# Optimization experiments

Hardware: AMD Instinct MI355X
Metric: run time of the kernel (lower is better)

The kernel has to match this reference:

```python
import jax, jax.numpy as jnp
import numpy as np
from math import sqrt

D_MODEL = 1024
N_HEADS = 16
D_V = D_MODEL // N_HEADS
D_FF = 4 * D_MODEL
EPS = 1e-5


def setup_inputs() -> dict:
    key = jax.random.key(0)
    ks = jax.random.split(key, 12)
    N, L = 2, 2048
    s = 0.02
    return {
        'queries': jax.random.normal(ks[0], (N, L, D_MODEL), jnp.float32),
        'keys': jax.random.normal(ks[1], (N, L, D_MODEL), jnp.float32),
        'values': jax.random.normal(ks[2], (N, L, D_MODEL), jnp.float32),
        'mask': jnp.ones((N, 1, 1, L), jnp.int32),
        'fc_w': jax.random.normal(ks[3], (D_MODEL, D_MODEL), jnp.float32) * s,
        'fc_b': jnp.zeros((D_MODEL,), jnp.float32),
        'ln1_g': jnp.ones((D_MODEL,), jnp.float32),
        'ln1_b': jnp.zeros((D_MODEL,), jnp.float32),
        'ff_w1': jax.random.normal(ks[4], (D_MODEL, D_FF), jnp.float32) * s,
        'ff_b1': jnp.zeros((D_FF,), jnp.float32),
        'ff_w2': jax.random.normal(ks[5], (D_FF, D_MODEL), jnp.float32) * s,
        'ff_b2': jnp.zeros((D_MODEL,), jnp.float32),
        'ln2_g': jnp.ones((D_MODEL,), jnp.float32),
        'ln2_b': jnp.zeros((D_MODEL,), jnp.float32),
    }


def layer_norm(x, g, b):
    mu = jnp.mean(x, axis=-1, keepdims=True)
    var = jnp.mean(jnp.square(x - mu), axis=-1, keepdims=True)
    return (x - mu) * jax.lax.rsqrt(var + EPS) * g + b


def reference(queries, keys, values, mask, fc_w, fc_b, ln1_g, ln1_b,
              ff_w1, ff_b1, ff_w2, ff_b2, ln2_g, ln2_b):
    N, Lq, _ = queries.shape
    Lk = keys.shape[1]
    # NOTE: the original module never applies its Q/K/V linear layers; raw
    # inputs are reshaped directly into heads.
    q = queries.reshape(N, Lq, N_HEADS, D_V).transpose(0, 2, 1, 3)  # nhqd
    k = keys.reshape(N, Lk, N_HEADS, D_V)                           # nlhd
    v = values.reshape(N, Lk, N_HEADS, D_V)                         # nlhd
    energy = jnp.einsum('nhqd,nlhd->nhql', q, k)
    energy = jnp.where(mask == 0, -jnp.inf, energy)
    # original scales by sqrt(d_model), not sqrt(d_v)
    attn = jax.nn.softmax(energy / sqrt(D_MODEL), axis=-1)
    out = jnp.einsum('nhql,nlhd->nqhd', attn, v).reshape(N, Lq, D_MODEL)
    attention = out @ fc_w + fc_b
    x1 = layer_norm(attention + queries, ln1_g, ln1_b)
    fc = jax.nn.relu(x1 @ ff_w1 + ff_b1) @ ff_w2 + ff_b2
    x2 = layer_norm(fc + x1, ln2_g, ln2_b)
    return x2
```

## Files before the change

### kernel.cpp

```cpp
#include <hip/hip_runtime.h>
#include <stdint.h>

typedef unsigned short u16;
typedef __bf16 bf16x8 __attribute__((ext_vector_type(8), may_alias));
typedef float f32x4 __attribute__((ext_vector_type(4), may_alias));

typedef void __attribute__((address_space(1))) as1_void;
typedef void __attribute__((address_space(3))) as3_void;

#define MFMA16 __builtin_amdgcn_mfma_f32_16x16x32_bf16

#define SBAR()                                \
    do {                                      \
        asm volatile("" ::: "memory");        \
        __builtin_amdgcn_s_barrier();         \
        asm volatile("" ::: "memory");        \
    } while (0)
#define WAITV(n) asm volatile("s_waitcnt vmcnt(" #n ")" ::: "memory")
#define WAITL0() asm volatile("s_waitcnt lgkmcnt(0)" ::: "memory")

__device__ __forceinline__ void async_copy16(const void* g, void* l) {
    __builtin_amdgcn_global_load_lds((as1_void*)g, (as3_void*)l, 16, 0, 0);
}

__device__ __forceinline__ u16 f2bf(float f) {
    union { float f; unsigned u; } c; c.f = f;
    unsigned u = c.u;
    u += 0x7fffu + ((u >> 16) & 1u);
    return (u16)(u >> 16);
}

__global__ __launch_bounds__(256) void cast_f32_bf16(
    const float* __restrict__ in, u16* __restrict__ out, int n4, float scale) {
    int i = blockIdx.x * 256 + threadIdx.x;
    if (i < n4) {
        f32x4 v = *(const f32x4*)&in[(size_t)i * 4];
        ushort4 o;
        o.x = f2bf(v[0] * scale); o.y = f2bf(v[1] * scale);
        o.z = f2bf(v[2] * scale); o.w = f2bf(v[3] * scale);
        *(ushort4*)&out[(size_t)i * 4] = o;
    }
}

__global__ __launch_bounds__(256) void transpose_cast(
    const float* __restrict__ in, u16* __restrict__ out, int R, int C) {
    __shared__ float tile[64][65];
    const float* inb = in + (size_t)blockIdx.z * R * C;
    u16* outb = out + (size_t)blockIdx.z * R * C;
    int t = threadIdx.x;
    int c0 = blockIdx.x * 64, r0 = blockIdx.y * 64;
    int tr = t >> 4, tc = (t & 15) * 4;
#pragma unroll
    for (int p = 0; p < 4; ++p) {
        int r = tr + p * 16;
        f32x4 v = *(const f32x4*)&inb[(size_t)(r0 + r) * C + c0 + tc];
        tile[r][tc] = v[0]; tile[r][tc + 1] = v[1];
        tile[r][tc + 2] = v[2]; tile[r][tc + 3] = v[3];
    }
    __syncthreads();
    int wc = t >> 4, wr = (t & 15) * 4;
#pragma unroll
    for (int p = 0; p < 4; ++p) {
        int cl = wc + p * 16;
        ushort4 o;
        o.x = f2bf(tile[wr + 0][cl]); o.y = f2bf(tile[wr + 1][cl]);
        o.z = f2bf(tile[wr + 2][cl]); o.w = f2bf(tile[wr + 3][cl]);
        *(ushort4*)&outb[(size_t)(c0 + cl) * R + r0 + wr] = o;
    }
}

__global__ __launch_bounds__(256) void flash_attn(
    const u16* __restrict__ Q, const u16* __restrict__ Kb,
    const u16* __restrict__ VT, const int* __restrict__ mask,
    u16* __restrict__ O) {
    __shared__ u16 kls[2][8192];
    __shared__ u16 vls[8192];
    __shared__ u16 pls[8][2048];

    const int bid = blockIdx.x;
    const int qt = bid & 15;
    const int h = (bid >> 4) & 15;
    const int n = bid >> 8;
    const int t = threadIdx.x;
    const int w = t >> 6, lane = t & 63;
    const int m16 = lane & 15, quad = lane >> 4;

    const size_t qrowA = (size_t)(n * 2048 + qt * 128 + w * 16 + m16);
    const size_t qrowB = qrowA + 64;
    bf16x8 qfA0 = *(const bf16x8*)&Q[qrowA * 1024 + h * 64 + quad * 8];
    bf16x8 qfA1 = *(const bf16x8*)&Q[qrowA * 1024 + h * 64 + 32 + quad * 8];
    bf16x8 qfB0 = *(const bf16x8*)&Q[qrowB * 1024 + h * 64 + quad * 8];
    bf16x8 qfB1 = *(const bf16x8*)&Q[qrowB * 1024 + h * 64 + 32 + quad * 8];

    const int* maskn = mask + n * 2048;
    int allones;
    {
        int ok = 1;
#pragma unroll
        for (int i = 0; i < 8; ++i) {
            int4 mv = *(const int4*)&maskn[lane * 32 + i * 4];
            ok &= (mv.x != 0) & (mv.y != 0) & (mv.z != 0) & (mv.w != 0);
        }
        allones = __all(ok);
    }

    f32x4 otA[4] = {}, otB[4] = {};
    f32x4 sumA = {}, sumB = {};

    const u16* Kbase = Kb + (size_t)(n * 2048) * 1024 + h * 64;
    const u16* Vbase = VT + (size_t)(n * 1024 + h * 64) * 2048;
    u16* pwA = &pls[w * 2][0];
    u16* pwB = &pls[w * 2 + 1][0];

#pragma unroll
    for (int i = 0; i < 4; ++i) {
        int e = w * 4 + i;
        async_copy16(&Kbase[(size_t)((e >> 1) * 16 + m16) * 1024 + (e & 1) * 32 + quad * 8],
                     &kls[0][e * 512]);
    }
    __syncthreads();

    for (int kt = 0; kt < 16; ++kt) {
        const u16* kcur = kls[kt & 1];
        if (kt + 1 < 16) {
            u16* knext = kls[(kt + 1) & 1];
#pragma unroll
            for (int i = 0; i < 4; ++i) {
                int e = w * 4 + i;
                async_copy16(&Kbase[(size_t)((kt + 1) * 128 + (e >> 1) * 16 + m16) * 1024 +
                                    (e & 1) * 32 + quad * 8], &knext[e * 512]);
            }
        }
#pragma unroll
        for (int i = 0; i < 4; ++i) {
            int e = w * 4 + i;
            async_copy16(&Vbase[(size_t)((e >> 2) * 16 + m16) * 2048 + kt * 128 +
                                (e & 3) * 32 + quad * 8], &vls[e * 512]);
        }

        f32x4 sA[8] = {}, sB[8] = {};
#pragma unroll
        for (int ct = 0; ct < 8; ++ct) {
            bf16x8 a0 = *(const bf16x8*)&kcur[(ct * 2 + 0) * 512 + lane * 8];
            bf16x8 a1 = *(const bf16x8*)&kcur[(ct * 2 + 1) * 512 + lane * 8];
            sA[ct] = MFMA16(a0, qfA0, sA[ct], 0, 0, 0);
            sA[ct] = MFMA16(a1, qfA1, sA[ct], 0, 0, 0);
            sB[ct] = MFMA16(a0, qfB0, sB[ct], 0, 0, 0);
            sB[ct] = MFMA16(a1, qfB1, sB[ct], 0, 0, 0);
        }

        if (allones) {
#pragma unroll
            for (int ct = 0; ct < 8; ++ct) {
                int c = ct * 2 + (quad >> 1);
                int off = m16 * 128 + (((c ^ m16) & 15) << 3) + (quad & 1) * 4;
                {
                    float p0 = __builtin_amdgcn_exp2f(sA[ct][0]);
                    float p1 = __builtin_amdgcn_exp2f(sA[ct][1]);
                    float p2 = __builtin_amdgcn_exp2f(sA[ct][2]);
                    float p3 = __builtin_amdgcn_exp2f(sA[ct][3]);
                    sumA[0] += p0; sumA[1] += p1; sumA[2] += p2; sumA[3] += p3;
                    unsigned lo = __builtin_amdgcn_perm(__float_as_uint(p1), __float_as_uint(p0), 0x07060302);
                    unsigned hi = __builtin_amdgcn_perm(__float_as_uint(p3), __float_as_uint(p2), 0x07060302);
                    *(uint2*)&pwA[off] = make_uint2(lo, hi);
                }
                {
                    float p0 = __builtin_amdgcn_exp2f(sB[ct][0]);
                    float p1 = __builtin_amdgcn_exp2f(sB[ct][1]);
                    float p2 = __builtin_amdgcn_exp2f(sB[ct][2]);
                    float p3 = __builtin_amdgcn_exp2f(sB[ct][3]);
                    sumB[0] += p0; sumB[1] += p1; sumB[2] += p2; sumB[3] += p3;
                    unsigned lo = __builtin_amdgcn_perm(__float_as_uint(p1), __float_as_uint(p0), 0x07060302);
                    unsigned hi = __builtin_amdgcn_perm(__float_as_uint(p3), __float_as_uint(p2), 0x07060302);
                    *(uint2*)&pwB[off] = make_uint2(lo, hi);
                }
            }
        } else {
#pragma unroll
            for (int ct = 0; ct < 8; ++ct) {
                const int4 mv = *(const int4*)&maskn[kt * 128 + ct * 16 + quad * 4];
                int c = ct * 2 + (quad >> 1);
                int off = m16 * 128 + (((c ^ m16) & 15) << 3) + (quad & 1) * 4;
                {
                    float p0 = __builtin_amdgcn_exp2f(sA[ct][0]) * (mv.x ? 1.f : 0.f);
                    float p1 = __builtin_amdgcn_exp2f(sA[ct][1]) * (mv.y ? 1.f : 0.f);
                    float p2 = __builtin_amdgcn_exp2f(sA[ct][2]) * (mv.z ? 1.f : 0.f);
                    float p3 = __builtin_amdgcn_exp2f(sA[ct][3]) * (mv.w ? 1.f : 0.f);
                    sumA[0] += p0; sumA[1] += p1; sumA[2] += p2; sumA[3] += p3;
                    unsigned lo = __builtin_amdgcn_perm(__float_as_uint(p1), __float_as_uint(p0), 0x07060302);
                    unsigned hi = __builtin_amdgcn_perm(__float_as_uint(p3), __float_as_uint(p2), 0x07060302);
                    *(uint2*)&pwA[off] = make_uint2(lo, hi);
                }
                {
                    float p0 = __builtin_amdgcn_exp2f(sB[ct][0]) * (mv.x ? 1.f : 0.f);
                    float p1 = __builtin_amdgcn_exp2f(sB[ct][1]) * (mv.y ? 1.f : 0.f);
                    float p2 = __builtin_amdgcn_exp2f(sB[ct][2]) * (mv.z ? 1.f : 0.f);
                    float p3 = __builtin_amdgcn_exp2f(sB[ct][3]) * (mv.w ? 1.f : 0.f);
                    sumB[0] += p0; sumB[1] += p1; sumB[2] += p2; sumB[3] += p3;
                    unsigned lo = __builtin_amdgcn_perm(__float_as_uint(p1), __float_as_uint(p0), 0x07060302);
                    unsigned hi = __builtin_amdgcn_perm(__float_as_uint(p3), __float_as_uint(p2), 0x07060302);
                    *(uint2*)&pwB[off] = make_uint2(lo, hi);
                }
            }
        }

        __syncthreads();

        bf16x8 pfA[4], pfB[4];
#pragma unroll
        for (int kc2 = 0; kc2 < 4; ++kc2) {
            int off = m16 * 128 + ((((kc2 * 4 + quad) ^ m16) & 15) << 3);
            pfA[kc2] = *(const bf16x8*)&pwA[off];
            pfB[kc2] = *(const bf16x8*)&pwB[off];
        }
#pragma unroll
        for (int kc2 = 0; kc2 < 4; ++kc2) {
#pragma unroll
            for (int dt = 0; dt < 4; ++dt) {
                bf16x8 vf = *(const bf16x8*)&vls[(dt * 4 + kc2) * 512 + lane * 8];
                otA[dt] = MFMA16(vf, pfA[kc2], otA[dt], 0, 0, 0);
                otB[dt] = MFMA16(vf, pfB[kc2], otB[dt], 0, 0, 0);
            }
        }
        __syncthreads();
    }

    float lA = (sumA[0] + sumA[1]) + (sumA[2] + sumA[3]);
    float lB = (sumB[0] + sumB[1]) + (sumB[2] + sumB[3]);
    lA += __shfl_xor(lA, 16); lA += __shfl_xor(lA, 32);
    lB += __shfl_xor(lB, 16); lB += __shfl_xor(lB, 32);
    float invA = 1.f / fmaxf(lA, 1e-30f);
    float invB = 1.f / fmaxf(lB, 1e-30f);

    const size_t obA = qrowA * 1024 + h * 64;
    const size_t obB = qrowB * 1024 + h * 64;
#pragma unroll
    for (int dt = 0; dt < 4; ++dt) {
        unsigned lo = (unsigned)f2bf(otA[dt][0] * invA) | ((unsigned)f2bf(otA[dt][1] * invA) << 16);
        unsigned hi = (unsigned)f2bf(otA[dt][2] * invA) | ((unsigned)f2bf(otA[dt][3] * invA) << 16);
        *(uint2*)&O[obA + dt * 16 + quad * 4] = make_uint2(lo, hi);
        lo = (unsigned)f2bf(otB[dt][0] * invB) | ((unsigned)f2bf(otB[dt][1] * invB) << 16);
        hi = (unsigned)f2bf(otB[dt][2] * invB) | ((unsigned)f2bf(otB[dt][3] * invB) << 16);
        *(uint2*)&O[obB + dt * 16 + quad * 4] = make_uint2(lo, hi);
    }
}

template <int BM, int BN, int RELU, int OUTBF, int SPLITK>
__global__ __launch_bounds__(256) void gemm_bt(
    const u16* __restrict__ A, const u16* __restrict__ Bt,
    const float* __restrict__ bias, void* __restrict__ Cout,
    void* __restrict__ Cout1, int M, int N, int K) {
    constexpr int MI = BM / 32;
    constexpr int NJ = BN / 32;
    __shared__ u16 sm[2][(BM + BN) * 64];
    const int lane = threadIdx.x & 63;
    const int w = threadIdx.x >> 6;
    const int m16 = lane & 15, quad = lane >> 4;
    const int nBn = N / BN;
    int bid = blockIdx.x;
    int slice = 0;
    if (SPLITK > 1) {
        const int nblk = (M / BM) * nBn;
        slice = bid / nblk;
        bid = bid - slice * nblk;
    }
    const int bm = bid / nBn, bn = bid % nBn;
    const int r2 = w >> 1, c2 = w & 1;
    const int Ks = K / SPLITK;
    const int kOff = slice * Ks;

    const u16* Abase = A + (size_t)(bm * BM + m16) * K + quad * 8;
    const u16* Bbase = Bt + (size_t)(bn * BN + m16) * K + quad * 8;

    auto stage = [&](int buf, int k0) {
        u16* smA = &sm[buf][0];
        u16* smB = smA + BM * 64;
#pragma unroll
        for (int i = 0; i < MI; ++i) {
            int e = w * MI + i;
            async_copy16(&Abase[(size_t)((e >> 1) * 16) * K + k0 + (e & 1) * 32], &smA[e * 512]);
        }
#pragma unroll
        for (int i = 0; i < NJ; ++i) {
            int e = w * NJ + i;
            async_copy16(&Bbase[(size_t)((e >> 1) * 16) * K + k0 + (e & 1) * 32], &smB[e * 512]);
        }
    };

    f32x4 acc[MI][NJ] = {};
    const int nK = Ks >> 6;
    stage(0, kOff);
    __syncthreads();
    for (int kt = 0; kt < nK; ++kt) {
        if (kt + 1 < nK) stage((kt + 1) & 1, kOff + ((kt + 1) << 6));
        const u16* smA = &sm[kt & 1][0];
        const u16* smB = smA + BM * 64;
#pragma unroll
        for (int kc = 0; kc < 2; ++kc) {
            bf16x8 a[MI], b[NJ];
#pragma unroll
            for (int i = 0; i < MI; ++i)
                a[i] = *(const bf16x8*)&smA[((r2 * MI + i) * 2 + kc) * 512 + lane * 8];
#pragma unroll
            for (int j = 0; j < NJ; ++j)
                b[j] = *(const bf16x8*)&smB[((c2 * NJ + j) * 2 + kc) * 512 + lane * 8];
#pragma unroll
            for (int i = 0; i < MI; ++i)
#pragma unroll
                for (int j = 0; j < NJ; ++j)
                    acc[i][j] = MFMA16(a[i], b[j], acc[i][j], 0, 0, 0);
        }
        __syncthreads();
    }
    float bv[NJ];
#pragma unroll
    for (int j = 0; j < NJ; ++j)
        bv[j] = (SPLITK == 1 || slice == 0)
                    ? bias[bn * BN + c2 * (BN / 2) + j * 16 + m16] : 0.f;
    void* Csel = (SPLITK > 1 && slice != 0) ? Cout1 : Cout;
#pragma unroll
    for (int i = 0; i < MI; ++i) {
        int row0 = bm * BM + r2 * (BM / 2) + i * 16 + quad * 4;
#pragma unroll
        for (int j = 0; j < NJ; ++j) {
            int col = bn * BN + c2 * (BN / 2) + j * 16 + m16;
#pragma unroll
            for (int r = 0; r < 4; ++r) {
                float v = acc[i][j][r] + bv[j];
                if (RELU) v = fmaxf(v, 0.f);
                size_t idx = (size_t)(row0 + r) * N + col;
                if (OUTBF) ((u16*)Csel)[idx] = f2bf(v);
                else ((float*)Csel)[idx] = v;
            }
        }
    }
}

template <int RELU, int OUTBF>
__global__ __launch_bounds__(512, 2) void gemm_8ph(
    const u16* __restrict__ A, const u16* __restrict__ Bt,
    const float* __restrict__ bias, void* __restrict__ Cout,
    int M, int N, int K) {
    __shared__ u16 sm[2][2][16384];
    const int t = threadIdx.x;
    const int w = t >> 6, lane = t & 63;
    const int m16 = lane & 15, quad = lane >> 4;
    const int wm = w >> 2, wn = w & 3;
    const int nBn = N >> 8;
    const int bid = blockIdx.x;
    const int bm = bid / nBn, bn = bid % nBn;
    const int nK = K >> 6, nIter = nK >> 1;
    const u16* Abase = A + (size_t)(bm * 256 + m16) * K + quad * 8;
    const u16* Bbase = Bt + (size_t)(bn * 256 + m16) * K + quad * 8;

    auto stage_ht = [&](int kt, int part) {
        if (kt < nK) {
            const u16* base = (part < 2) ? Abase : Bbase;
            u16* lds = &sm[kt & 1][part >> 1][0];
#pragma unroll
            for (int i = 0; i < 2; ++i) {
                int e;
                if (part == 0)      e = i * 16 + w;
                else if (part == 1) e = 8 + i * 16 + w;
                else if (part == 2) e = i * 8 + w;
                else                e = 16 + i * 8 + w;
                async_copy16(&base[(size_t)((e >> 1) * 16) * K + (size_t)kt * 64 + (e & 1) * 32],
                             &lds[e * 512]);
            }
        }
    };
    auto ldsA = [&](int buf, int mf, int kc) {
        return *(const bf16x8*)&sm[buf][0][((wm * 8 + mf) * 2 + kc) * 512 + lane * 8];
    };
    auto ldsB = [&](int buf, int nf, int kc) {
        return *(const bf16x8*)&sm[buf][1][((wn * 4 + nf) * 2 + kc) * 512 + lane * 8];
    };

    f32x4 acc[8][4] = {};
    bf16x8 a0[4][2], a1[4][2], b[4][2];

#define QUAD8(Ar, BO, MO)                                                       \
    do {                                                                        \
        __builtin_amdgcn_s_setprio(1);                                          \
        _Pragma("unroll") for (int mi = 0; mi < 4; ++mi)                        \
            _Pragma("unroll") for (int nj = 0; nj < 2; ++nj)                    \
                _Pragma("unroll") for (int kc = 0; kc < 2; ++kc)                \
                    acc[(MO) + mi][(BO) + nj] =                                 \
                        MFMA16(Ar[mi][kc], b[(BO) + nj][kc],                    \
                               acc[(MO) + mi][(BO) + nj], 0, 0, 0);             \
        __builtin_amdgcn_s_setprio(0);                                          \
    } while (0)

    stage_ht(0, 0); stage_ht(0, 1); stage_ht(0, 2); stage_ht(0, 3);
    stage_ht(1, 0); stage_ht(1, 1); stage_ht(1, 2);
    WAITV(6);
    SBAR();

    for (int it = 0; it < nIter; ++it) {
        const int T1 = 2 * it + 1, T2 = 2 * it + 2, T3 = 2 * it + 3;
        const bool last = (it + 1 == nIter);
#pragma unroll
        for (int mf = 0; mf < 4; ++mf) { a0[mf][0] = ldsA(0, mf, 0); a0[mf][1] = ldsA(0, mf, 1); }
#pragma unroll
        for (int nf = 0; nf < 2; ++nf) { b[nf][0] = ldsB(0, nf, 0); b[nf][1] = ldsB(0, nf, 1); }
        stage_ht(T1, 3);
        SBAR(); WAITL0();
        QUAD8(a0, 0, 0);
        SBAR();
#pragma unroll
        for (int mf = 0; mf < 4; ++mf) { a1[mf][0] = ldsA(0, mf + 4, 0); a1[mf][1] = ldsA(0, mf + 4, 1); }
#pragma unroll
        for (int nf = 0; nf < 2; ++nf) { b[2 + nf][0] = ldsB(0, 2 + nf, 0); b[2 + nf][1] = ldsB(0, 2 + nf, 1); }
        stage_ht(T2, 0);
        SBAR(); WAITL0();
        QUAD8(a0, 2, 0);
        SBAR();
        stage_ht(T2, 1);
        SBAR(); WAITL0();
        QUAD8(a1, 2, 4);
        SBAR();
        stage_ht(T2, 2);
        if (last) { WAITV(0); } else { WAITV(6); }
        SBAR(); WAITL0();
        QUAD8(a1, 0, 4);
        SBAR();
#pragma unroll
        for (int mf = 0; mf < 4; ++mf) { a0[mf][0] = ldsA(1, mf, 0); a0[mf][1] = ldsA(1, mf, 1); }
#pragma unroll
        for (int nf = 0; nf < 2; ++nf) { b[nf][0] = ldsB(1, nf, 0); b[nf][1] = ldsB(1, nf, 1); }
        stage_ht(T2, 3);
        SBAR(); WAITL0();
        QUAD8(a0, 0, 0);
        SBAR();
#pragma unroll
        for (int mf = 0; mf < 4; ++mf) { a1[mf][0] = ldsA(1, mf + 4, 0); a1[mf][1] = ldsA(1, mf + 4, 1); }
#pragma unroll
        for (int nf = 0; nf < 2; ++nf) { b[2 + nf][0] = ldsB(1, 2 + nf, 0); b[2 + nf][1] = ldsB(1, 2 + nf, 1); }
        stage_ht(T3, 0);
        SBAR(); WAITL0();
        QUAD8(a0, 2, 0);
        SBAR();
        stage_ht(T3, 1);
        SBAR(); WAITL0();
        QUAD8(a1, 2, 4);
        SBAR();
        stage_ht(T3, 2);
        if (last) { WAITV(0); } else { WAITV(6); }
        SBAR(); WAITL0();
        QUAD8(a1, 0, 4);
        SBAR();
    }
#undef QUAD8

    float bv[4];
#pragma unroll
    for (int nf = 0; nf < 4; ++nf)
        bv[nf] = bias[bn * 256 + wn * 64 + nf * 16 + m16];
    const int colb = bn * 256 + wn * 64 + m16;
#pragma unroll
    for (int mf = 0; mf < 8; ++mf) {
        const int row0 = bm * 256 + wm * 128 + mf * 16 + quad * 4;
#pragma unroll
        for (int nf = 0; nf < 4; ++nf) {
#pragma unroll
            for (int r = 0; r < 4; ++r) {
                float vv = acc[mf][nf][r] + bv[nf];
                if (RELU) vv = fmaxf(vv, 0.f);
                size_t idx = (size_t)(row0 + r) * N + colb + nf * 16;
                if (OUTBF) ((u16*)Cout)[idx] = f2bf(vv);
                else ((float*)Cout)[idx] = vv;
            }
        }
    }
}

template <int RELU, int OUTBF, int SPLITK>
__global__ __launch_bounds__(512, 2) void gemm_sk(
    const u16* __restrict__ A, const u16* __restrict__ Bt,
    const float* __restrict__ bias,
    void* __restrict__ C0, void* __restrict__ C1,
    int M, int N, int K) {
    __shared__ u16 smA[2][8192];
    __shared__ u16 smB[2][16384];
    const int t = threadIdx.x;
    const int w = t >> 6, lane = t & 63;
    const int m16 = lane & 15, quad = lane >> 4;
    const int wm = w >> 2, wn = w & 3;
    const int nBn = N >> 8;
    const int nblk = (M >> 7) * nBn * SPLITK;
    const int o = blockIdx.x;
    const int v = (o & 7) * (nblk >> 3) + (o >> 3);
    const int gsz = nBn * SPLITK;
    const int bm = v / gsz;
    const int rr = v - bm * gsz;
    const int slice = rr / nBn;
    const int bn = rr - slice * nBn;
    const int Ks = K / SPLITK;
    const int nK = Ks >> 6, nIter = nK >> 1;
    const u16* Abase = A + (size_t)(bm * 128 + m16) * K + slice * Ks + quad * 8;
    const u16* Bbase = Bt + (size_t)(bn * 256 + m16) * K + slice * Ks + quad * 8;

    auto stage_u = [&](int kt, int part) {
        if (kt < nK) {
#pragma unroll
            for (int i = 0; i < 2; ++i) {
                const int idx = i * 8 + w;
                int e;
                const u16* base;
                u16* lds;
                if (part == 0) {
                    e = idx; base = Abase; lds = &smA[kt & 1][0];
                } else {
                    const int rbs = idx >> 1;
                    const int rb = ((rbs >> 1) << 2) | (rbs & 1) | ((part == 2) ? 2 : 0);
                    e = rb * 2 + (idx & 1);
                    base = Bbase; lds = &smB[kt & 1][0];
                }
                async_copy16(&base[(size_t)((e >> 1) * 16) * K + (size_t)kt * 64 + (e & 1) * 32],
                             &lds[e * 512]);
            }
        }
    };
    auto ldsA = [&](int buf, int mf, int kc) {
        return *(const bf16x8*)&smA[buf][((wm * 4 + mf) * 2 + kc) * 512 + lane * 8];
    };
    auto ldsB = [&](int buf, int nf, int kc) {
        return *(const bf16x8*)&smB[buf][((wn * 4 + nf) * 2 + kc) * 512 + lane * 8];
    };

    f32x4 acc[4][4] = {};
    bf16x8 af[4][2], bf[2][2];

#define QUADS(NO)                                                               \
    do {                                                                        \
        __builtin_amdgcn_s_setprio(1);                                          \
        _Pragma("unroll") for (int mi = 0; mi < 4; ++mi)                        \
            _Pragma("unroll") for (int nj = 0; nj < 2; ++nj)                    \
                _Pragma("unroll") for (int kc = 0; kc < 2; ++kc)                \
                    acc[mi][(NO) + nj] =                                        \
                        MFMA16(af[mi][kc], bf[nj][kc],                          \
                               acc[mi][(NO) + nj], 0, 0, 0);                    \
        __builtin_amdgcn_s_setprio(0);                                          \
    } while (0)

    stage_u(0, 0); stage_u(0, 1); stage_u(0, 2);
    stage_u(1, 0); stage_u(1, 1);
    WAITV(4);
    SBAR();

    for (int it = 0; it < nIter; ++it) {
        const int T1 = 2 * it + 1, T2 = 2 * it + 2, T3 = 2 * it + 3;
        const bool last = (it + 1 == nIter);
#pragma unroll
        for (int mf = 0; mf < 4; ++mf) { af[mf][0] = ldsA(0, mf, 0); af[mf][1] = ldsA(0, mf, 1); }
#pragma unroll
        for (int nf = 0; nf < 2; ++nf) { bf[nf][0] = ldsB(0, nf, 0); bf[nf][1] = ldsB(0, nf, 1); }
        stage_u(T1, 2);
        SBAR(); WAITL0();
        QUADS(0);
        SBAR();
#pragma unroll
        for (int nf = 0; nf < 2; ++nf) { bf[nf][0] = ldsB(0, 2 + nf, 0); bf[nf][1] = ldsB(0, 2 + nf, 1); }
        stage_u(T2, 0); stage_u(T2, 1);
        if (last) { WAITV(0); } else { WAITV(4); }
        SBAR(); WAITL0();
        QUADS(2);
        SBAR();
#pragma unroll
        for (int mf = 0; mf < 4; ++mf) { af[mf][0] = ldsA(1, mf, 0); af[mf][1] = ldsA(1, mf, 1); }
#pragma unroll
        for (int nf = 0; nf < 2; ++nf) { bf[nf][0] = ldsB(1, nf, 0); bf[nf][1] = ldsB(1, nf, 1); }
        stage_u(T2, 2);
        SBAR(); WAITL0();
        QUADS(0);
        SBAR();
#pragma unroll
        for (int nf = 0; nf < 2; ++nf) { bf[nf][0] = ldsB(1, 2 + nf, 0); bf[nf][1] = ldsB(1, 2 + nf, 1); }
        stage_u(T3, 0); stage_u(T3, 1);
        if (last) { WAITV(0); } else { WAITV(4); }
        SBAR(); WAITL0();
        QUADS(2);
        SBAR();
    }
#undef QUADS

    float bv[4];
#pragma unroll
    for (int nf = 0; nf < 4; ++nf)
        bv[nf] = (SPLITK == 1 || slice == 0)
                     ? bias[bn * 256 + wn * 64 + nf * 16 + m16] : 0.f;
    void* Csel = (SPLITK > 1 && slice != 0) ? C1 : C0;
    const int colb = bn * 256 + wn * 64 + m16;
#pragma unroll
    for (int mf = 0; mf < 4; ++mf) {
        const int row0 = bm * 128 + wm * 64 + mf * 16 + quad * 4;
#pragma unroll
        for (int nf = 0; nf < 4; ++nf) {
#pragma unroll
            for (int r = 0; r < 4; ++r) {
                float vv = acc[mf][nf][r] + bv[nf];
                if (RELU) vv = fmaxf(vv, 0.f);
                size_t idx = (size_t)(row0 + r) * N + colb + nf * 16;
                if (OUTBF) ((u16*)Csel)[idx] = f2bf(vv);
                else ((float*)Csel)[idx] = vv;
            }
        }
    }
}

__global__ __launch_bounds__(256) void ln_residual(
    const float* __restrict__ x, const float* x2,
    const float* __restrict__ res,
    const float* __restrict__ g, const float* __restrict__ b,
    float* __restrict__ out_f32, u16* __restrict__ out_bf16) {
    __shared__ float smr[8];
    int row = blockIdx.x;
    int t = threadIdx.x;
    f32x4 xv = *(const f32x4*)&x[(size_t)row * 1024 + t * 4];
    f32x4 rv = *(const f32x4*)&res[(size_t)row * 1024 + t * 4];
    xv += rv;
    if (x2) xv += *(const f32x4*)&x2[(size_t)row * 1024 + t * 4];
    float s = xv[0] + xv[1] + xv[2] + xv[3];
    float ss = xv[0] * xv[0] + xv[1] * xv[1] + xv[2] * xv[2] + xv[3] * xv[3];
#pragma unroll
    for (int d = 1; d < 64; d <<= 1) {
        s += __shfl_xor(s, d);
        ss += __shfl_xor(ss, d);
    }
    int w = t >> 6, lane = t & 63;
    if (lane == 0) { smr[w] = s; smr[4 + w] = ss; }
    __syncthreads();
    s = smr[0] + smr[1] + smr[2] + smr[3];
    ss = smr[4] + smr[5] + smr[6] + smr[7];
    float mu = s * (1.f / 1024.f);
    float var = ss * (1.f / 1024.f) - mu * mu;
    float rs = rsqrtf(var + 1e-5f);
    f32x4 gv = *(const f32x4*)&g[t * 4];
    f32x4 bv = *(const f32x4*)&b[t * 4];
    f32x4 y;
#pragma unroll
    for (int i = 0; i < 4; ++i) y[i] = (xv[i] - mu) * rs * gv[i] + bv[i];
    *(f32x4*)&out_f32[(size_t)row * 1024 + t * 4] = y;
    if (out_bf16) {
        ushort4 o;
        o.x = f2bf(y[0]); o.y = f2bf(y[1]); o.z = f2bf(y[2]); o.w = f2bf(y[3]);
        *(ushort4*)&out_bf16[(size_t)row * 1024 + t * 4] = o;
    }
}

extern "C" void kernel_launch(void* const* d_in, const int* in_sizes, int n_in,
                              void* d_out, int out_size, void* d_ws, size_t ws_size,
                              hipStream_t stream) {
    const float* q = (const float*)d_in[0];
    const float* k = (const float*)d_in[1];
    const float* v = (const float*)d_in[2];
    const int* mask = (const int*)d_in[3];
    const float* fc_b = (const float*)d_in[5];
    const float* ln1_g = (const float*)d_in[6];
    const float* ln1_b = (const float*)d_in[7];
    const float* ff_b1 = (const float*)d_in[9];
    const float* ff_b2 = (const float*)d_in[11];
    const float* ln2_g = (const float*)d_in[12];
    const float* ln2_b = (const float*)d_in[13];
    const float* fc_w = (const float*)d_in[4];
    const float* ff_w1 = (const float*)d_in[8];
    const float* ff_w2 = (const float*)d_in[10];

    char* ws = (char*)d_ws;
    const size_t MB = 1024 * 1024;
    u16* qbf = (u16*)(ws + 0);
    u16* kbf = (u16*)(ws + 8 * MB);
    u16* vT  = (u16*)(ws + 16 * MB);
    u16* ao  = (u16*)(ws + 24 * MB);
    u16* hbuf = (u16*)(ws + 0);
    u16* fcwT = (u16*)(ws + 32 * MB);
    u16* w1T  = (u16*)(ws + 34 * MB);
    u16* w2T  = (u16*)(ws + 42 * MB);
    float* attn_raw = (float*)(ws + 50 * MB);
    float* fc_raw   = (float*)(ws + 50 * MB);
    float* x1   = (float*)(ws + 66 * MB);
    u16* x1bf   = (u16*)(ws + 82 * MB);
    float* attn_rawB = (float*)(ws + 0);
    float* fcB  = (float*)(ws + 90 * MB);
    const bool big = ws_size >= 106 * MB;

    const float k2 = 0.03125f * 1.44269504088896340736f;

    cast_f32_bf16<<<4096, 256, 0, stream>>>(q, qbf, 1048576, k2);
    cast_f32_bf16<<<4096, 256, 0, stream>>>(k, kbf, 1048576, 1.0f);
    transpose_cast<<<dim3(16, 32, 2), 256, 0, stream>>>(v, vT, 2048, 1024);
    transpose_cast<<<dim3(16, 16, 1), 256, 0, stream>>>(fc_w, fcwT, 1024, 1024);
    transpose_cast<<<dim3(64, 16, 1), 256, 0, stream>>>(ff_w1, w1T, 1024, 4096);
    transpose_cast<<<dim3(16, 64, 1), 256, 0, stream>>>(ff_w2, w2T, 4096, 1024);

    flash_attn<<<512, 256, 0, stream>>>(qbf, kbf, vT, mask, ao);

    gemm_sk<0, 0, 2><<<256, 512, 0, stream>>>(
        ao, fcwT, fc_b, attn_raw, attn_rawB, 4096, 1024, 1024);
    ln_residual<<<4096, 256, 0, stream>>>(attn_raw, attn_rawB, q, ln1_g, ln1_b, x1, x1bf);

    gemm_8ph<1, 1><<<256, 512, 0, stream>>>(
        x1bf, w1T, ff_b1, hbuf, 4096, 4096, 1024);

    if (big) {
        gemm_sk<0, 0, 2><<<256, 512, 0, stream>>>(
            hbuf, w2T, ff_b2, fc_raw, fcB, 4096, 1024, 4096);
        ln_residual<<<4096, 256, 0, stream>>>(fc_raw, fcB, x1, ln2_g, ln2_b,
                                              (float*)d_out, (u16*)nullptr);
    } else {
        gemm_bt<64, 128, 0, 0, 1><<<64 * 8, 256, 0, stream>>>(
            hbuf, w2T, ff_b2, fc_raw, nullptr, 4096, 1024, 4096);
        ln_residual<<<4096, 256, 0, stream>>>(fc_raw, nullptr, x1, ln2_g, ln2_b,
                                              (float*)d_out, (u16*)nullptr);
    }
}
```

Before: 370.0 us.

## Software-pipeline LDS fragment reads with partial lgkmcnt waits in GEMM loops

Both GEMM main loops now issue LDS reads for the next quad's A/B fragments before running the current MFMA quad, using separate even/odd register sets and partial lgkmcnt waits instead of waiting for all LDS traffic. The goal is to overlap LDS read latency with MFMA execution and drop a few barrier-separated phases. This raises register pressure, and the correctness of the hand-counted lgkmcnt values depends on how the compiler orders the instructions.

```diff
diff --git a/kernel.cpp b/kernel.cpp
--- a/kernel.cpp
+++ b/kernel.cpp
@@ -17,7 +17,7 @@
         asm volatile("" ::: "memory");        \
     } while (0)
 #define WAITV(n) asm volatile("s_waitcnt vmcnt(" #n ")" ::: "memory")
-#define WAITL0() asm volatile("s_waitcnt lgkmcnt(0)" ::: "memory")
+#define WAITL(n) asm volatile("s_waitcnt lgkmcnt(" #n ")" ::: "memory")
 
 __device__ __forceinline__ void async_copy16(const void* g, void* l) {
     __builtin_amdgcn_global_load_lds((as1_void*)g, (as3_void*)l, 16, 0, 0);
@@ -377,17 +377,32 @@
     };
 
     f32x4 acc[8][4] = {};
-    bf16x8 a0[4][2], a1[4][2], b[4][2];
-
-#define QUAD8(Ar, BO, MO)                                                       \
+    bf16x8 a0[4][2], a1[4][2], b01E[2][2], b01O[2][2], b23[2][2];
+
+#define RD_A0(buf)                                                              \
+    _Pragma("unroll") for (int mf = 0; mf < 4; ++mf) {                          \
+        a0[mf][0] = ldsA(buf, mf, 0); a0[mf][1] = ldsA(buf, mf, 1); }
+#define RD_A1(buf)                                                              \
+    _Pragma("unroll") for (int mf = 0; mf < 4; ++mf) {                          \
+        a1[mf][0] = ldsA(buf, mf + 4, 0); a1[mf][1] = ldsA(buf, mf + 4, 1); }
+#define RD_B01E(buf)                                                            \
+    _Pragma("unroll") for (int nf = 0; nf < 2; ++nf) {                          \
+        b01E[nf][0] = ldsB(buf, nf, 0); b01E[nf][1] = ldsB(buf, nf, 1); }
+#define RD_B01O(buf)                                                            \
+    _Pragma("unroll") for (int nf = 0; nf < 2; ++nf) {                          \
+        b01O[nf][0] = ldsB(buf, nf, 0); b01O[nf][1] = ldsB(buf, nf, 1); }
+#define RD_B23(buf)                                                             \
+    _Pragma("unroll") for (int nf = 0; nf < 2; ++nf) {                          \
+        b23[nf][0] = ldsB(buf, 2 + nf, 0); b23[nf][1] = ldsB(buf, 2 + nf, 1); }
+#define QUAD8(Ar, Br, MO, NO)                                                   \
     do {                                                                        \
         __builtin_amdgcn_s_setprio(1);                                          \
         _Pragma("unroll") for (int mi = 0; mi < 4; ++mi)                        \
             _Pragma("unroll") for (int nj = 0; nj < 2; ++nj)                    \
                 _Pragma("unroll") for (int kc = 0; kc < 2; ++kc)                \
-                    acc[(MO) + mi][(BO) + nj] =                                 \
-                        MFMA16(Ar[mi][kc], b[(BO) + nj][kc],                    \
-                               acc[(MO) + mi][(BO) + nj], 0, 0, 0);             \
+                    acc[(MO) + mi][(NO) + nj] =                                 \
+                        MFMA16(Ar[mi][kc], Br[nj][kc],                          \
+                               acc[(MO) + mi][(NO) + nj], 0, 0, 0);             \
         __builtin_amdgcn_s_setprio(0);                                          \
     } while (0)
 
@@ -395,62 +410,54 @@
     stage_ht(1, 0); stage_ht(1, 1); stage_ht(1, 2);
     WAITV(6);
     SBAR();
+    RD_A0(0); RD_B01E(0);
 
     for (int it = 0; it < nIter; ++it) {
         const int T1 = 2 * it + 1, T2 = 2 * it + 2, T3 = 2 * it + 3;
         const bool last = (it + 1 == nIter);
-#pragma unroll
-        for (int mf = 0; mf < 4; ++mf) { a0[mf][0] = ldsA(0, mf, 0); a0[mf][1] = ldsA(0, mf, 1); }
-#pragma unroll
-        for (int nf = 0; nf < 2; ++nf) { b[nf][0] = ldsB(0, nf, 0); b[nf][1] = ldsB(0, nf, 1); }
-        stage_ht(T1, 3);
-        SBAR(); WAITL0();
-        QUAD8(a0, 0, 0);
-        SBAR();
-#pragma unroll
-        for (int mf = 0; mf < 4; ++mf) { a1[mf][0] = ldsA(0, mf + 4, 0); a1[mf][1] = ldsA(0, mf + 4, 1); }
-#pragma unroll
-        for (int nf = 0; nf < 2; ++nf) { b[2 + nf][0] = ldsB(0, 2 + nf, 0); b[2 + nf][1] = ldsB(0, 2 + nf, 1); }
-        stage_ht(T2, 0);
-        SBAR(); WAITL0();
-        QUAD8(a0, 2, 0);
-        SBAR();
-        stage_ht(T2, 1);
-        SBAR(); WAITL0();
-        QUAD8(a1, 2, 4);
-        SBAR();
-        stage_ht(T2, 2);
+        RD_B23(0); stage_ht(T1, 3);
+        SBAR(); WAITL(4);
+        QUAD8(a0, b01E, 0, 0);
+        SBAR();
+        RD_A1(0); stage_ht(T2, 0);
+        SBAR(); WAITL(8);
+        QUAD8(a0, b23, 0, 2);
+        SBAR();
+        WAITL(0);
+        QUAD8(a1, b23, 4, 2);
+        SBAR();
+        stage_ht(T2, 1); stage_ht(T2, 2);
         if (last) { WAITV(0); } else { WAITV(6); }
-        SBAR(); WAITL0();
-        QUAD8(a1, 0, 4);
-        SBAR();
-#pragma unroll
-        for (int mf = 0; mf < 4; ++mf) { a0[mf][0] = ldsA(1, mf, 0); a0[mf][1] = ldsA(1, mf, 1); }
-#pragma unroll
-        for (int nf = 0; nf < 2; ++nf) { b[nf][0] = ldsB(1, nf, 0); b[nf][1] = ldsB(1, nf, 1); }
-        stage_ht(T2, 3);
-        SBAR(); WAITL0();
-        QUAD8(a0, 0, 0);
-        SBAR();
-#pragma unroll
-        for (int mf = 0; mf < 4; ++mf) { a1[mf][0] = ldsA(1, mf + 4, 0); a1[mf][1] = ldsA(1, mf + 4, 1); }
-#pragma unroll
-        for (int nf = 0; nf < 2; ++nf) { b[2 + nf][0] = ldsB(1, 2 + nf, 0); b[2 + nf][1] = ldsB(1, 2 + nf, 1); }
-        stage_ht(T3, 0);
-        SBAR(); WAITL0();
-        QUAD8(a0, 2, 0);
-        SBAR();
-        stage_ht(T3, 1);
-        SBAR(); WAITL0();
-        QUAD8(a1, 2, 4);
-        SBAR();
-        stage_ht(T3, 2);
+        SBAR();
+        RD_A0(1); RD_B01O(1);
+        WAITL(12);
+        QUAD8(a1, b01E, 4, 0);
+        SBAR();
+        RD_B23(1); stage_ht(T2, 3);
+        SBAR(); WAITL(4);
+        QUAD8(a0, b01O, 0, 0);
+        SBAR();
+        RD_A1(1); stage_ht(T3, 0);
+        SBAR(); WAITL(8);
+        QUAD8(a0, b23, 0, 2);
+        SBAR();
+        WAITL(0);
+        QUAD8(a1, b23, 4, 2);
+        SBAR();
+        stage_ht(T3, 1); stage_ht(T3, 2);
         if (last) { WAITV(0); } else { WAITV(6); }
-        SBAR(); WAITL0();
-        QUAD8(a1, 0, 4);
+        SBAR();
+        if (!last) { RD_A0(0); RD_B01E(0); }
+        WAITL(12);
+        QUAD8(a1, b01O, 4, 0);
         SBAR();
     }
 #undef QUAD8
+#undef RD_A0
+#undef RD_A1
+#undef RD_B01E
+#undef RD_B01O
+#undef RD_B23
 
     float bv[4];
 #pragma unroll
@@ -529,16 +536,28 @@
     };
 
     f32x4 acc[4][4] = {};
-    bf16x8 af[4][2], bf[2][2];
-
-#define QUADS(NO)                                                               \
+    bf16x8 afE[4][2], afO[4][2], al[2][2], be[2][2];
+
+#define RD_AFE(buf)                                                             \
+    _Pragma("unroll") for (int mf = 0; mf < 4; ++mf) {                          \
+        afE[mf][0] = ldsA(buf, mf, 0); afE[mf][1] = ldsA(buf, mf, 1); }
+#define RD_AFO(buf)                                                             \
+    _Pragma("unroll") for (int mf = 0; mf < 4; ++mf) {                          \
+        afO[mf][0] = ldsA(buf, mf, 0); afO[mf][1] = ldsA(buf, mf, 1); }
+#define RD_AL(buf)                                                              \
+    _Pragma("unroll") for (int nf = 0; nf < 2; ++nf) {                          \
+        al[nf][0] = ldsB(buf, nf, 0); al[nf][1] = ldsB(buf, nf, 1); }
+#define RD_BE(buf)                                                              \
+    _Pragma("unroll") for (int nf = 0; nf < 2; ++nf) {                          \
+        be[nf][0] = ldsB(buf, 2 + nf, 0); be[nf][1] = ldsB(buf, 2 + nf, 1); }
+#define QUADS(Ar, Br, NO)                                                       \
     do {                                                                        \
         __builtin_amdgcn_s_setprio(1);                                          \
         _Pragma("unroll") for (int mi = 0; mi < 4; ++mi)                        \
             _Pragma("unroll") for (int nj = 0; nj < 2; ++nj)                    \
                 _Pragma("unroll") for (int kc = 0; kc < 2; ++kc)                \
                     acc[mi][(NO) + nj] =                                        \
-                        MFMA16(af[mi][kc], bf[nj][kc],                          \
+                        MFMA16(Ar[mi][kc], Br[nj][kc],                          \
                                acc[mi][(NO) + nj], 0, 0, 0);                    \
         __builtin_amdgcn_s_setprio(0);                                          \
     } while (0)
@@ -547,42 +566,39 @@
     stage_u(1, 0); stage_u(1, 1);
     WAITV(4);
     SBAR();
+    RD_AFE(0); RD_AL(0);
 
     for (int it = 0; it < nIter; ++it) {
         const int T1 = 2 * it + 1, T2 = 2 * it + 2, T3 = 2 * it + 3;
         const bool last = (it + 1 == nIter);
-#pragma unroll
-        for (int mf = 0; mf < 4; ++mf) { af[mf][0] = ldsA(0, mf, 0); af[mf][1] = ldsA(0, mf, 1); }
-#pragma unroll
-        for (int nf = 0; nf < 2; ++nf) { bf[nf][0] = ldsB(0, nf, 0); bf[nf][1] = ldsB(0, nf, 1); }
-        stage_u(T1, 2);
-        SBAR(); WAITL0();
-        QUADS(0);
-        SBAR();
-#pragma unroll
-        for (int nf = 0; nf < 2; ++nf) { bf[nf][0] = ldsB(0, 2 + nf, 0); bf[nf][1] = ldsB(0, 2 + nf, 1); }
+        RD_BE(0); stage_u(T1, 2);
+        SBAR(); WAITL(4);
+        QUADS(afE, al, 0);
+        SBAR();
         stage_u(T2, 0); stage_u(T2, 1);
         if (last) { WAITV(0); } else { WAITV(4); }
-        SBAR(); WAITL0();
-        QUADS(2);
-        SBAR();
-#pragma unroll
-        for (int mf = 0; mf < 4; ++mf) { af[mf][0] = ldsA(1, mf, 0); af[mf][1] = ldsA(1, mf, 1); }
-#pragma unroll
-        for (int nf = 0; nf < 2; ++nf) { bf[nf][0] = ldsB(1, nf, 0); bf[nf][1] = ldsB(1, nf, 1); }
-        stage_u(T2, 2);
-        SBAR(); WAITL0();
-        QUADS(0);
-        SBAR();
-#pragma unroll
-        for (int nf = 0; nf < 2; ++nf) { bf[nf][0] = ldsB(1, 2 + nf, 0); bf[nf][1] = ldsB(1, 2 + nf, 1); }
+        SBAR();
+        RD_AFO(1); RD_AL(1);
+        WAITL(12);
+        QUADS(afE, be, 2);
+        SBAR();
+        RD_BE(1); stage_u(T2, 2);
+        SBAR(); WAITL(4);
+        QUADS(afO, al, 0);
+        SBAR();
         stage_u(T3, 0); stage_u(T3, 1);
         if (last) { WAITV(0); } else { WAITV(4); }
-        SBAR(); WAITL0();
-        QUADS(2);
+        SBAR();
+        if (!last) { RD_AFE(0); RD_AL(0); }
+        WAITL(12);
+        QUADS(afO, be, 2);
         SBAR();
     }
 #undef QUADS
+#undef RD_AFE
+#undef RD_AFO
+#undef RD_AL
+#undef RD_BE
 
     float bv[4];
 #pragma unroll
```

New measurement: 395.0 us. 6.8% more time.
